# Kernel tuning notes

Hardware: AMD Instinct MI355X
Metric: run time of the kernel (lower is better)

## Reference

```python
import jax, jax.numpy as jnp
import numpy as np

# Dims: batch, queries, graph nodes, text len, hidden, heads, layers, ffn
B, NQ, NN, T, D, H, LAYERS, FF = 16, 32, 128, 352, 768, 8, 6, 3072
L = NQ + NN + T          # 512 total sequence length
HD = D // H              # 96 head dim
NEG = -1e9               # additive mask value (HF uses dtype min; -1e9 is equivalent post-softmax)
LN_EPS = 1e-12           # BERT LayerNorm eps


def _ln(x, g, b):
    m = x.mean(-1, keepdims=True)
    v = ((x - m) ** 2).mean(-1, keepdims=True)
    return (x - m) * jax.lax.rsqrt(v + LN_EPS) * g + b


def setup_inputs() -> dict:
    key = jax.random.key(0)
    ks = iter(jax.random.split(key, 32))

    def nrm(shape, s=0.02):
        return jax.random.normal(next(ks), shape, jnp.float32) * s

    return {
        "graph_node_features": jax.random.normal(next(ks), (B, NN, D), jnp.float32),
        "text_embeds": jax.random.normal(next(ks), (B, T, D), jnp.float32),
        "text_atts": jnp.ones((B, T), jnp.int32),
        "graph_mask": jnp.ones((B, NN), jnp.int32),
        "query_tokens": nrm((1, NQ, D), 1.0),   # nn.Parameter(torch.randn(...))
        "gproj_w": nrm((D, D)), "gproj_b": jnp.zeros((D,)),
        "pos_emb": nrm((L, D)), "tok_emb": nrm((D,)),  # token_type row 0
        "emb_ln_g": jnp.ones((D,)), "emb_ln_b": jnp.zeros((D,)),
        "qkv_w": nrm((LAYERS, D, 3 * D)), "qkv_b": jnp.zeros((LAYERS, 3 * D)),
        "ao_w": nrm((LAYERS, D, D)), "ao_b": jnp.zeros((LAYERS, D)),
        "ln1_g": jnp.ones((LAYERS, D)), "ln1_b": jnp.zeros((LAYERS, D)),
        "ff1_w": nrm((LAYERS, D, FF)), "ff1_b": jnp.zeros((LAYERS, FF)),
        "ff2_w": nrm((LAYERS, FF, D)), "ff2_b": jnp.zeros((LAYERS, D)),
        "ln2_g": jnp.ones((LAYERS, D)), "ln2_b": jnp.zeros((LAYERS, D)),
    }


def _itg_bias(text_atts, graph_mask):
    # Build the custom ITG prefix-LM mask: bidirectional over [queries|graph],
    # causal over text, and queries/graph blocked from attending to text.
    keep = jnp.concatenate(
        [jnp.ones((B, NQ), jnp.int32), graph_mask, text_atts], axis=1)  # [B, L]
    ts = NQ + NN
    idx = jnp.arange(L)
    is_text = idx >= ts
    pair = (keep[:, :, None] * keep[:, None, :]).astype(bool)          # padding mask
    causal_ok = jnp.where(is_text[:, None] & is_text[None, :],
                          idx[:, None] >= idx[None, :], True)           # tril in text block
    block_ok = ~((~is_text)[:, None] & is_text[None, :])                # prefix cannot see text
    mask = pair & causal_ok & block_ok                                  # [B, L, L]
    return jnp.where(mask, 0.0, NEG)[:, None, :, :]                     # [B, 1, L, L]


def reference(graph_node_features, text_embeds, text_atts, graph_mask,
              query_tokens, gproj_w, gproj_b, pos_emb, tok_emb,
              emb_ln_g, emb_ln_b, qkv_w, qkv_b, ao_w, ao_b,
              ln1_g, ln1_b, ff1_w, ff1_b, ff2_w, ff2_b, ln2_g, ln2_b):
    gfeat = graph_node_features @ gproj_w + gproj_b
    qtok = jnp.broadcast_to(query_tokens, (B, NQ, D))
    x = jnp.concatenate([qtok, gfeat, text_embeds], axis=1)             # [B, L, D]
    bias = _itg_bias(text_atts, graph_mask)

    # BERT embeddings (inputs_embeds path): + position + token_type(0), LN (dropout off)
    x = _ln(x + pos_emb[None] + tok_emb, emb_ln_g, emb_ln_b)

    scale = 1.0 / np.sqrt(HD)
    for i in range(LAYERS):
        qkv = x @ qkv_w[i] + qkv_b[i]
        q, k, v = jnp.split(qkv, 3, axis=-1)
        q = q.reshape(B, L, H, HD)
        k = k.reshape(B, L, H, HD)
        v = v.reshape(B, L, H, HD)
        s = jnp.einsum('bqhd,bkhd->bhqk', q, k) * scale + bias
        p = jax.nn.softmax(s, axis=-1)
        ctx = jnp.einsum('bhqk,bkhd->bqhd', p, v).reshape(B, L, D)
        x = _ln(x + ctx @ ao_w[i] + ao_b[i], ln1_g[i], ln1_b[i])
        h = jax.nn.gelu(x @ ff1_w[i] + ff1_b[i], approximate=False)
        x = _ln(x + h @ ff2_w[i] + ff2_b[i], ln2_g[i], ln2_b[i])

    return x[:, NQ + NN:, :]   # text_feats [B, T, D]
```

## Files before the change

### kernel.cpp

```cpp
#include <hip/hip_runtime.h>
#include <math.h>

typedef __bf16 bf16;
typedef __bf16 bf16x8 __attribute__((ext_vector_type(8)));
typedef float f32x4 __attribute__((ext_vector_type(4)));

#define NQ   32
#define NN_  128
#define TT   352
#define DD   768
#define NH   8
#define HDIM 96
#define LSEQ 512
#define TSPLIT 160
#define FFD  3072
#define NLAYER 6
#define NBATCH 16

template <int ACT>
__global__ __launch_bounds__(256) void gemm_bt(
    const bf16* __restrict__ A, const bf16* __restrict__ Bt,
    bf16* __restrict__ C, const float* __restrict__ bias,
    int K, int lda, int ldb, int ldc, float alpha, int Nstore)
{
    __shared__ __attribute__((aligned(16))) bf16 As[128 * 32];
    __shared__ __attribute__((aligned(16))) bf16 Bs[128 * 32];

    const int n0 = blockIdx.x * 128, m0 = blockIdx.y * 128;
    const int t = threadIdx.x;
    const int w = t >> 6, l = t & 63;
    const int wm = w >> 1, wn = w & 1;
    const int lr = l & 15, quad = l >> 4;

    f32x4 acc[4][4] = {};

    const int f0 = w * 1024 + l * 8;
    const int ra0 = f0 >> 5, ca0 = f0 & 31;
    const int ra1 = (f0 + 512) >> 5, ca1 = (f0 + 512) & 31;
    bf16* ldsA0 = &As[w * 1024];
    bf16* ldsA1 = &As[w * 1024 + 512];
    bf16* ldsB0 = &Bs[w * 1024];
    bf16* ldsB1 = &Bs[w * 1024 + 512];
    const bf16* a0 = A  + (size_t)(m0 + ra0) * lda + ca0;
    const bf16* a1 = A  + (size_t)(m0 + ra1) * lda + ca1;
    const bf16* b0 = Bt + (size_t)(n0 + ra0) * ldb + ca0;
    const bf16* b1 = Bt + (size_t)(n0 + ra1) * ldb + ca1;

    for (int k0 = 0; k0 < K; k0 += 32) {
        __syncthreads();
        __builtin_amdgcn_global_load_lds(
            (const __attribute__((address_space(1))) void*)(a0 + k0),
            (__attribute__((address_space(3))) void*)ldsA0, 16, 0, 0);
        __builtin_amdgcn_global_load_lds(
            (const __attribute__((address_space(1))) void*)(a1 + k0),
            (__attribute__((address_space(3))) void*)ldsA1, 16, 0, 0);
        __builtin_amdgcn_global_load_lds(
            (const __attribute__((address_space(1))) void*)(b0 + k0),
            (__attribute__((address_space(3))) void*)ldsB0, 16, 0, 0);
        __builtin_amdgcn_global_load_lds(
            (const __attribute__((address_space(1))) void*)(b1 + k0),
            (__attribute__((address_space(3))) void*)ldsB1, 16, 0, 0);
        __syncthreads();

        bf16x8 af[4], bf_[4];
#pragma unroll
        for (int i = 0; i < 4; ++i)
            af[i] = *(const bf16x8*)&As[(wm * 64 + i * 16 + lr) * 32 + quad * 8];
#pragma unroll
        for (int j = 0; j < 4; ++j)
            bf_[j] = *(const bf16x8*)&Bs[(wn * 64 + j * 16 + lr) * 32 + quad * 8];
#pragma unroll
        for (int i = 0; i < 4; ++i)
#pragma unroll
            for (int j = 0; j < 4; ++j)
                acc[i][j] = __builtin_amdgcn_mfma_f32_16x16x32_bf16(af[i], bf_[j], acc[i][j], 0, 0, 0);
    }

#pragma unroll
    for (int i = 0; i < 4; ++i) {
        const int grow = m0 + wm * 64 + i * 16 + quad * 4;
#pragma unroll
        for (int j = 0; j < 4; ++j) {
            const int gcol = n0 + wn * 64 + j * 16 + lr;
            if (gcol >= Nstore) continue;
            float bv = bias ? bias[gcol] : 0.0f;
#pragma unroll
            for (int r = 0; r < 4; ++r) {
                float v = acc[i][j][r] * alpha + bv;
                if (ACT == 1) v = 0.5f * v * (1.0f + erff(v * 0.70710678118654752f));
                C[(size_t)(grow + r) * ldc + gcol] = (bf16)v;
            }
        }
    }
}

__global__ __launch_bounds__(256) void flash_attn(
    const bf16* __restrict__ qkv, bf16* __restrict__ ctx,
    const int* __restrict__ tatts, const int* __restrict__ gmask)
{
    __shared__ __attribute__((aligned(16))) bf16 Qs[64 * 104];
    __shared__ __attribute__((aligned(16))) bf16 Ks[64 * 104];
    __shared__ __attribute__((aligned(16))) bf16 Vs[96 * 72];
    __shared__ __attribute__((aligned(16))) bf16 Ps[64 * 72];
    __shared__ int keep[512];

    const int qt = blockIdx.x;
    const int bh = blockIdx.y;
    const int b = bh >> 3, h = bh & 7;
    const int q0 = qt * 64;
    const int t = threadIdx.x;
    const int w = t >> 6, l = t & 63;
    const int lr = l & 15, quad = l >> 4;
    const float scale = 0.10206207261596577f;

    const bf16* qbase = qkv + (size_t)b * 512 * 2304 + h * 96;
    const bf16* kbase = qbase + 768;
    const bf16* vbase = qbase + 1536;

    for (int j = t; j < 512; j += 256)
        keep[j] = (j < NQ) ? 1 : (j < TSPLIT ? gmask[b * NN_ + j - NQ]
                                             : tatts[b * TT + j - TSPLIT]);

#pragma unroll
    for (int c = 0; c < 3; ++c) {
        const int idx = t * 8 + c * 2048;
        const int r = idx / 96, d = idx % 96;
        *(bf16x8*)&Qs[r * 104 + d] =
            *(const bf16x8*)&qbase[(size_t)(q0 + r) * 2304 + d];
    }
    __syncthreads();

    int ki[4];
    int ig[4];
#pragma unroll
    for (int r = 0; r < 4; ++r) {
        ig[r] = q0 + w * 16 + quad * 4 + r;
        ki[r] = keep[ig[r]];
    }

    float m_run[4] = {-1e30f, -1e30f, -1e30f, -1e30f};
    float l_run[4] = {0.f, 0.f, 0.f, 0.f};
    f32x4 oc[6] = {};

    const int JMAX = (qt < 3) ? 128 : q0;
    for (int j0 = 0; j0 <= JMAX; j0 += 64) {
        __syncthreads();
#pragma unroll
        for (int c = 0; c < 3; ++c) {
            const int idx = t * 8 + c * 2048;
            const int r = idx / 96, d = idx % 96;
            *(bf16x8*)&Ks[r * 104 + d] =
                *(const bf16x8*)&kbase[(size_t)(j0 + r) * 2304 + d];
            bf16x8 vv = *(const bf16x8*)&vbase[(size_t)(j0 + r) * 2304 + d];
#pragma unroll
            for (int jj = 0; jj < 8; ++jj)
                Vs[(d + jj) * 72 + r] = vv[jj];
        }
        __syncthreads();

        bf16x8 aq[3];
#pragma unroll
        for (int ds = 0; ds < 3; ++ds)
            aq[ds] = *(const bf16x8*)&Qs[(w * 16 + lr) * 104 + ds * 32 + quad * 8];
        f32x4 sc[4];
#pragma unroll
        for (int cb = 0; cb < 4; ++cb) {
            f32x4 a = {};
#pragma unroll
            for (int ds = 0; ds < 3; ++ds) {
                bf16x8 bk = *(const bf16x8*)&Ks[(cb * 16 + lr) * 104 + ds * 32 + quad * 8];
                a = __builtin_amdgcn_mfma_f32_16x16x32_bf16(aq[ds], bk, a, 0, 0, 0);
            }
            sc[cb] = a;
        }

        float tm[4] = {-1e30f, -1e30f, -1e30f, -1e30f};
#pragma unroll
        for (int cb = 0; cb < 4; ++cb) {
            const int jg = j0 + cb * 16 + lr;
            const int kj = keep[jg];
#pragma unroll
            for (int r = 0; r < 4; ++r) {
                const int i = ig[r];
                bool ok = ki[r] && kj;
                if (i < TSPLIT && jg >= TSPLIT) ok = false;
                if (i >= TSPLIT && jg >= TSPLIT && i < jg) ok = false;
                float s = sc[cb][r] * scale + (ok ? 0.f : -1e9f);
                sc[cb][r] = s;
                tm[r] = fmaxf(tm[r], s);
            }
        }
#pragma unroll
        for (int off = 1; off < 16; off <<= 1)
#pragma unroll
            for (int r = 0; r < 4; ++r)
                tm[r] = fmaxf(tm[r], __shfl_xor(tm[r], off));

        float alpha_[4], ts[4] = {0.f, 0.f, 0.f, 0.f};
#pragma unroll
        for (int r = 0; r < 4; ++r) {
            const float mn = fmaxf(m_run[r], tm[r]);
            alpha_[r] = __expf(m_run[r] - mn);
            m_run[r] = mn;
            l_run[r] *= alpha_[r];
        }
#pragma unroll
        for (int db = 0; db < 6; ++db)
#pragma unroll
            for (int r = 0; r < 4; ++r)
                oc[db][r] *= alpha_[r];

#pragma unroll
        for (int cb = 0; cb < 4; ++cb)
#pragma unroll
            for (int r = 0; r < 4; ++r) {
                const float p = __expf(sc[cb][r] - m_run[r]);
                ts[r] += p;
                Ps[(w * 16 + quad * 4 + r) * 72 + cb * 16 + lr] = (bf16)p;
            }
#pragma unroll
        for (int off = 1; off < 16; off <<= 1)
#pragma unroll
            for (int r = 0; r < 4; ++r)
                ts[r] += __shfl_xor(ts[r], off);
#pragma unroll
        for (int r = 0; r < 4; ++r) l_run[r] += ts[r];

        __syncthreads();

#pragma unroll
        for (int l0 = 0; l0 < 64; l0 += 32) {
            bf16x8 ap = *(const bf16x8*)&Ps[(w * 16 + lr) * 72 + l0 + quad * 8];
#pragma unroll
            for (int db = 0; db < 6; ++db) {
                bf16x8 bv = *(const bf16x8*)&Vs[(db * 16 + lr) * 72 + l0 + quad * 8];
                oc[db] = __builtin_amdgcn_mfma_f32_16x16x32_bf16(ap, bv, oc[db], 0, 0, 0);
            }
        }
    }

#pragma unroll
    for (int r = 0; r < 4; ++r) {
        const float inv = 1.f / l_run[r];
        bf16* orow = ctx + ((size_t)b * 512 + ig[r]) * 768 + h * 96;
#pragma unroll
        for (int db = 0; db < 6; ++db)
            orow[db * 16 + lr] = (bf16)(oc[db][r] * inv);
    }
}

__global__ void transpose_w(const float* __restrict__ in, bf16* __restrict__ out,
                            int R, int C)
{
    __shared__ bf16 tile[32][33];
    const int c0 = blockIdx.x * 32, r0 = blockIdx.y * 32;
    const int tx = threadIdx.x & 31, ty = threadIdx.x >> 5;
    for (int i = ty; i < 32; i += 8)
        tile[i][tx] = (bf16)in[(size_t)(r0 + i) * C + c0 + tx];
    __syncthreads();
    for (int i = ty; i < 32; i += 8)
        out[(size_t)(c0 + i) * R + r0 + tx] = tile[tx][i];
}

__global__ void cvt_bf16(const float* __restrict__ in, bf16* __restrict__ out, int n)
{
    const int idx = blockIdx.x * 256 + threadIdx.x;
    if (idx < n) out[idx] = (bf16)in[idx];
}

__device__ __forceinline__ void block_reduce_2(float& a, float& b)
{
#pragma unroll
    for (int off = 32; off; off >>= 1) {
        a += __shfl_xor(a, off);
        b += __shfl_xor(b, off);
    }
    __shared__ float sa[4], sb[4];
    const int w = threadIdx.x >> 6;
    if ((threadIdx.x & 63) == 0) { sa[w] = a; sb[w] = b; }
    __syncthreads();
    a = sa[0] + sa[1] + sa[2] + sa[3];
    b = sb[0] + sb[1] + sb[2] + sb[3];
}

__global__ void embed_ln(const float* __restrict__ qtok, const bf16* __restrict__ gfeat,
                         const float* __restrict__ text, const float* __restrict__ pos,
                         const float* __restrict__ tok, const float* __restrict__ g,
                         const float* __restrict__ bb, bf16* __restrict__ x)
{
    const int row = blockIdx.x;
    const int l = row & 511, b = row >> 9;
    const int t = threadIdx.x;

    float vals[3], s = 0.f, sq = 0.f;
#pragma unroll
    for (int c = 0; c < 3; ++c) {
        const int d = t + c * 256;
        float base;
        if (l < NQ)           base = qtok[(size_t)l * DD + d];
        else if (l < TSPLIT)  base = (float)gfeat[((size_t)b * NN_ + (l - NQ)) * DD + d];
        else                  base = text[((size_t)b * TT + (l - TSPLIT)) * DD + d];
        float v = base + pos[(size_t)l * DD + d] + tok[d];
        vals[c] = v; s += v; sq += v * v;
    }
    block_reduce_2(s, sq);
    const float mean = s * (1.f / 768.f);
    const float var = sq * (1.f / 768.f) - mean * mean;
    const float rs = rsqrtf(var + 1e-12f);
    bf16* o = x + (size_t)row * DD;
#pragma unroll
    for (int c = 0; c < 3; ++c) {
        const int d = t + c * 256;
        o[d] = (bf16)((vals[c] - mean) * rs * g[d] + bb[d]);
    }
}

__global__ void ln_rows(const bf16* __restrict__ X, const bf16* __restrict__ Y,
                        bf16* __restrict__ Out, const float* __restrict__ g,
                        const float* __restrict__ bb)
{
    const int row = blockIdx.x;
    const int t = threadIdx.x;
    const bf16* xr = X + (size_t)row * DD;
    const bf16* yr = Y + (size_t)row * DD;
    float vals[3], s = 0.f, sq = 0.f;
#pragma unroll
    for (int c = 0; c < 3; ++c) {
        const int d = t + c * 256;
        float v = (float)xr[d] + (float)yr[d];
        vals[c] = v; s += v; sq += v * v;
    }
    block_reduce_2(s, sq);
    const float mean = s * (1.f / 768.f);
    const float var = sq * (1.f / 768.f) - mean * mean;
    const float rs = rsqrtf(var + 1e-12f);
    bf16* o = Out + (size_t)row * DD;
#pragma unroll
    for (int c = 0; c < 3; ++c) {
        const int d = t + c * 256;
        o[d] = (bf16)((vals[c] - mean) * rs * g[d] + bb[d]);
    }
}

__global__ void copy_out(const bf16* __restrict__ x, float* __restrict__ out)
{
    const size_t idx = (size_t)blockIdx.x * 256 + threadIdx.x;
    const int d = idx % DD;
    const size_t row = idx / DD;
    const int t = row % TT;
    const int b = row / TT;
    out[idx] = (float)x[((size_t)b * LSEQ + TSPLIT + t) * DD + d];
}

static void launch_gemm(const bf16* A, const bf16* Bt, bf16* C, const float* bias,
                        int M, int K, int lda, int ldb, int ldc,
                        float alpha, int Nstore, int act, hipStream_t stream)
{
    dim3 grid((Nstore + 127) / 128, M / 128, 1);
    if (act)
        gemm_bt<1><<<grid, 256, 0, stream>>>(A, Bt, C, bias, K, lda, ldb, ldc, alpha, Nstore);
    else
        gemm_bt<0><<<grid, 256, 0, stream>>>(A, Bt, C, bias, K, lda, ldb, ldc, alpha, Nstore);
}

extern "C" void kernel_launch(void* const* d_in, const int* in_sizes, int n_in,
                              void* d_out, int out_size, void* d_ws, size_t ws_size,
                              hipStream_t stream)
{
    const float* gnf     = (const float*)d_in[0];
    const float* text    = (const float*)d_in[1];
    const int*   tatts   = (const int*)d_in[2];
    const int*   gmask   = (const int*)d_in[3];
    const float* qtok    = (const float*)d_in[4];
    const float* gproj_w = (const float*)d_in[5];
    const float* gproj_b = (const float*)d_in[6];
    const float* pos     = (const float*)d_in[7];
    const float* tok     = (const float*)d_in[8];
    const float* eg      = (const float*)d_in[9];
    const float* eb      = (const float*)d_in[10];
    const float* qkv_w   = (const float*)d_in[11];
    const float* qkv_b   = (const float*)d_in[12];
    const float* ao_w    = (const float*)d_in[13];
    const float* ao_b    = (const float*)d_in[14];
    const float* ln1g    = (const float*)d_in[15];
    const float* ln1b    = (const float*)d_in[16];
    const float* ff1_w   = (const float*)d_in[17];
    const float* ff1_b   = (const float*)d_in[18];
    const float* ff2_w   = (const float*)d_in[19];
    const float* ff2_b   = (const float*)d_in[20];
    const float* ln2g    = (const float*)d_in[21];
    const float* ln2b    = (const float*)d_in[22];
    float* out = (float*)d_out;

    bf16* ws   = (bf16*)d_ws;
    bf16* wt1  = ws;
    bf16* wt2  = wt1 + 2359296;
    bf16* x    = wt2 + 2359296;
    bf16* ctx  = x   + 6291456;
    bf16* t1   = ctx + 6291456;
    bf16* u    = t1  + 6291456;
    bf16* qkvb = u;
    bf16* hbuf = u;
    bf16* gfeat = t1;
    bf16* gnfb  = u;

    dim3 blk(256);

    cvt_bf16<<<6144, blk, 0, stream>>>(gnf, gnfb, 1572864);
    transpose_w<<<dim3(24, 24), blk, 0, stream>>>(gproj_w, wt1, 768, 768);
    launch_gemm(gnfb, wt1, gfeat, gproj_b, 2048, 768, 768, 768, 768,
                1.f, 768, 0, stream);
    embed_ln<<<8192, blk, 0, stream>>>(qtok, gfeat, text, pos, tok, eg, eb, x);

    for (int i = 0; i < NLAYER; ++i) {
        transpose_w<<<dim3(72, 24), blk, 0, stream>>>(
            qkv_w + (size_t)i * 768 * 2304, wt1, 768, 2304);
        launch_gemm(x, wt1, qkvb, qkv_b + i * 2304,
                    8192, 768, 768, 768, 2304, 1.f, 2304, 0, stream);
        flash_attn<<<dim3(8, 128), blk, 0, stream>>>(qkvb, ctx, tatts, gmask);
        transpose_w<<<dim3(24, 24), blk, 0, stream>>>(
            ao_w + (size_t)i * 589824, wt1, 768, 768);
        launch_gemm(ctx, wt1, t1, ao_b + i * 768,
                    8192, 768, 768, 768, 768, 1.f, 768, 0, stream);
        ln_rows<<<8192, blk, 0, stream>>>(x, t1, x, ln1g + i * 768, ln1b + i * 768);

        transpose_w<<<dim3(96, 24), blk, 0, stream>>>(
            ff1_w + (size_t)i * 2359296, wt1, 768, 3072);
        transpose_w<<<dim3(24, 96), blk, 0, stream>>>(
            ff2_w + (size_t)i * 2359296, wt2, 3072, 768);
        launch_gemm(x, wt1, hbuf, ff1_b + i * 3072,
                    8192, 768, 768, 768, 3072, 1.f, 3072, 1, stream);
        launch_gemm(hbuf, wt2, t1, ff2_b + i * 768,
                    8192, 3072, 3072, 3072, 768, 1.f, 768, 0, stream);
        ln_rows<<<8192, blk, 0, stream>>>(x, t1, x, ln2g + i * 768, ln2b + i * 768);
    }

    copy_out<<<16896, blk, 0, stream>>>(x, out);

    (void)in_sizes; (void)n_in; (void)out_size; (void)ws_size;
}
```

Baseline: 2.313 ms.

## Swizzle GEMM LDS layout and remap workgroup IDs across XCDs

Applies an XOR swizzle to the LDS tiles of the bf16 GEMM. Global-to-LDS loads fetch permuted source addresses so that the MFMA fragment reads avoid bank conflicts. It also remaps the linear workgroup ID so consecutive tiles are grouped per XCD chunk, to improve L2 locality on the multi-die MI355X. The permutation must be consistent between the load and read sides, otherwise results are corrupted.

```diff
diff --git a/kernel.cpp b/kernel.cpp
--- a/kernel.cpp
+++ b/kernel.cpp
@@ -26,7 +26,15 @@
     __shared__ __attribute__((aligned(16))) bf16 As[128 * 32];
     __shared__ __attribute__((aligned(16))) bf16 Bs[128 * 32];
 
-    const int n0 = blockIdx.x * 128, m0 = blockIdx.y * 128;
+    const int nwg = gridDim.x * gridDim.y;
+    int id = blockIdx.y * gridDim.x + blockIdx.x;
+    if ((nwg & 7) == 0) {
+        const int chunk = nwg >> 3;
+        id = (id & 7) * chunk + (id >> 3);
+    }
+    const int bx = id % gridDim.x, by = id / gridDim.x;
+    const int n0 = bx * 128, m0 = by * 128;
+
     const int t = threadIdx.x;
     const int w = t >> 6, l = t & 63;
     const int wm = w >> 1, wn = w & 1;
@@ -34,17 +42,21 @@
 
     f32x4 acc[4][4] = {};
 
-    const int f0 = w * 1024 + l * 8;
-    const int ra0 = f0 >> 5, ca0 = f0 & 31;
-    const int ra1 = (f0 + 512) >> 5, ca1 = (f0 + 512) & 31;
+    const int G0 = w * 128 + l;
+    const int G1 = G0 + 64;
+    const int gd0 = G0 ^ (((G0 >> 2) & 7) ^ ((G0 >> 4) & 1));
+    const int gd1 = G1 ^ (((G1 >> 2) & 7) ^ ((G1 >> 4) & 1));
+    const int r0 = gd0 >> 2, c0 = (gd0 & 3) * 8;
+    const int r1 = gd1 >> 2, c1 = (gd1 & 3) * 8;
+
     bf16* ldsA0 = &As[w * 1024];
     bf16* ldsA1 = &As[w * 1024 + 512];
     bf16* ldsB0 = &Bs[w * 1024];
     bf16* ldsB1 = &Bs[w * 1024 + 512];
-    const bf16* a0 = A  + (size_t)(m0 + ra0) * lda + ca0;
-    const bf16* a1 = A  + (size_t)(m0 + ra1) * lda + ca1;
-    const bf16* b0 = Bt + (size_t)(n0 + ra0) * ldb + ca0;
-    const bf16* b1 = Bt + (size_t)(n0 + ra1) * ldb + ca1;
+    const bf16* a0 = A  + (size_t)(m0 + r0) * lda + c0;
+    const bf16* a1 = A  + (size_t)(m0 + r1) * lda + c1;
+    const bf16* b0 = Bt + (size_t)(n0 + r0) * ldb + c0;
+    const bf16* b1 = Bt + (size_t)(n0 + r1) * ldb + c1;
 
     for (int k0 = 0; k0 < K; k0 += 32) {
         __syncthreads();
@@ -64,11 +76,17 @@
 
         bf16x8 af[4], bf_[4];
 #pragma unroll
-        for (int i = 0; i < 4; ++i)
-            af[i] = *(const bf16x8*)&As[(wm * 64 + i * 16 + lr) * 32 + quad * 8];
-#pragma unroll
-        for (int j = 0; j < 4; ++j)
-            bf_[j] = *(const bf16x8*)&Bs[(wn * 64 + j * 16 + lr) * 32 + quad * 8];
+        for (int i = 0; i < 4; ++i) {
+            const int row = wm * 64 + i * 16 + lr;
+            const int eo = (row * 32 + quad * 8) ^ ((row & 7) << 3);
+            af[i] = *(const bf16x8*)&As[eo];
+        }
+#pragma unroll
+        for (int j = 0; j < 4; ++j) {
+            const int row = wn * 64 + j * 16 + lr;
+            const int eo = (row * 32 + quad * 8) ^ ((row & 7) << 3);
+            bf_[j] = *(const bf16x8*)&Bs[eo];
+        }
 #pragma unroll
         for (int i = 0; i < 4; ++i)
 #pragma unroll
```

Measured after the change: 2.224 ms. 1.04x faster.

## Double-buffer LDS tiles in bf16 GEMM to overlap global loads with MFMA

Applied to the files above, without the earlier changes.

The GEMM kernel now keeps two LDS buffers for the A and B tiles. It prefetches the next K-slice with global_load_lds into the spare buffer while running MFMAs on the current one, and drops one of the two barriers per iteration. This aims to hide global memory latency behind matrix math in the kernel that carries most of the work (QKV, output projection and FFN). In exchange the kernel uses twice the shared memory per block, which may lower occupancy. Correctness relies on the barrier at the top of each iteration also waiting for the outstanding LDS-direct loads to finish.

```diff
diff --git a/kernel.cpp b/kernel.cpp
--- a/kernel.cpp
+++ b/kernel.cpp
@@ -17,14 +17,19 @@
 #define NLAYER 6
 #define NBATCH 16
 
+#define GLOAD(srcp, dstp)                                                     \
+    __builtin_amdgcn_global_load_lds(                                         \
+        (const __attribute__((address_space(1))) void*)(srcp),                \
+        (__attribute__((address_space(3))) void*)(dstp), 16, 0, 0)
+
 template <int ACT>
 __global__ __launch_bounds__(256) void gemm_bt(
     const bf16* __restrict__ A, const bf16* __restrict__ Bt,
     bf16* __restrict__ C, const float* __restrict__ bias,
     int K, int lda, int ldb, int ldc, float alpha, int Nstore)
 {
-    __shared__ __attribute__((aligned(16))) bf16 As[128 * 32];
-    __shared__ __attribute__((aligned(16))) bf16 Bs[128 * 32];
+    __shared__ __attribute__((aligned(16))) bf16 As[2 * 128 * 32];
+    __shared__ __attribute__((aligned(16))) bf16 Bs[2 * 128 * 32];
 
     const int n0 = blockIdx.x * 128, m0 = blockIdx.y * 128;
     const int t = threadIdx.x;
@@ -37,38 +42,43 @@
     const int f0 = w * 1024 + l * 8;
     const int ra0 = f0 >> 5, ca0 = f0 & 31;
     const int ra1 = (f0 + 512) >> 5, ca1 = (f0 + 512) & 31;
-    bf16* ldsA0 = &As[w * 1024];
-    bf16* ldsA1 = &As[w * 1024 + 512];
-    bf16* ldsB0 = &Bs[w * 1024];
-    bf16* ldsB1 = &Bs[w * 1024 + 512];
     const bf16* a0 = A  + (size_t)(m0 + ra0) * lda + ca0;
     const bf16* a1 = A  + (size_t)(m0 + ra1) * lda + ca1;
     const bf16* b0 = Bt + (size_t)(n0 + ra0) * ldb + ca0;
     const bf16* b1 = Bt + (size_t)(n0 + ra1) * ldb + ca1;
 
-    for (int k0 = 0; k0 < K; k0 += 32) {
+    const int nt = K >> 5;
+
+    {
+        bf16* pA = &As[w * 1024];
+        bf16* pB = &Bs[w * 1024];
+        GLOAD(a0, pA);
+        GLOAD(a1, pA + 512);
+        GLOAD(b0, pB);
+        GLOAD(b1, pB + 512);
+    }
+
+    for (int tt = 0; tt < nt; ++tt) {
         __syncthreads();
-        __builtin_amdgcn_global_load_lds(
-            (const __attribute__((address_space(1))) void*)(a0 + k0),
-            (__attribute__((address_space(3))) void*)ldsA0, 16, 0, 0);
-        __builtin_amdgcn_global_load_lds(
-            (const __attribute__((address_space(1))) void*)(a1 + k0),
-            (__attribute__((address_space(3))) void*)ldsA1, 16, 0, 0);
-        __builtin_amdgcn_global_load_lds(
-            (const __attribute__((address_space(1))) void*)(b0 + k0),
-            (__attribute__((address_space(3))) void*)ldsB0, 16, 0, 0);
-        __builtin_amdgcn_global_load_lds(
-            (const __attribute__((address_space(1))) void*)(b1 + k0),
-            (__attribute__((address_space(3))) void*)ldsB1, 16, 0, 0);
-        __syncthreads();
+        const int cur = (tt & 1) << 12;
+        const int nxt = 4096 - cur;
+        if (tt + 1 < nt) {
+            const int k0 = (tt + 1) << 5;
+            bf16* pA = &As[nxt + w * 1024];
+            bf16* pB = &Bs[nxt + w * 1024];
+            GLOAD(a0 + k0, pA);
+            GLOAD(a1 + k0, pA + 512);
+            GLOAD(b0 + k0, pB);
+            GLOAD(b1 + k0, pB + 512);
+        }
 
         bf16x8 af[4], bf_[4];
 #pragma unroll
         for (int i = 0; i < 4; ++i)
-            af[i] = *(const bf16x8*)&As[(wm * 64 + i * 16 + lr) * 32 + quad * 8];
+            af[i] = *(const bf16x8*)&As[cur + (wm * 64 + i * 16 + lr) * 32 + quad * 8];
 #pragma unroll
         for (int j = 0; j < 4; ++j)
-            bf_[j] = *(const bf16x8*)&Bs[(wn * 64 + j * 16 + lr) * 32 + quad * 8];
+            bf_[j] = *(const bf16x8*)&Bs[cur + (wn * 64 + j * 16 + lr) * 32 + quad * 8];
 #pragma unroll
         for (int i = 0; i < 4; ++i)
 #pragma unroll
```

New measurement: 2.208 ms. -4.5%, faster.
